# Kernel tuning notes

Measured on AMD Instinct MI355X. Metric: run time of the kernel, lower is better.

Reference implementation:

```python
import jax, jax.numpy as jnp
import numpy as np

N = 50000      # nodes
E = 800000     # edges (before self loops)
D_IN = 128
HID = 64
HEADS = 8
D_OUT = 10


def setup_inputs() -> dict:
    key = jax.random.key(0)
    ks = jax.random.split(key, 16)
    sc = 0.05
    x = jax.random.normal(ks[0], (N, D_IN), dtype=jnp.float32)
    edge_index = jax.random.randint(ks[1], (2, E), 0, N, dtype=jnp.int64)
    return {
        "x": x,
        "edge_index": edge_index,
        "W1": jax.random.normal(ks[2], (HEADS * HID, D_IN), dtype=jnp.float32) * sc,
        "a1_src": jax.random.normal(ks[3], (HEADS, HID), dtype=jnp.float32) * sc,
        "a1_dst": jax.random.normal(ks[4], (HEADS, HID), dtype=jnp.float32) * sc,
        "b1": jnp.zeros((HEADS * HID,), jnp.float32),
        "W2": jax.random.normal(ks[5], (HID, HEADS * HID), dtype=jnp.float32) * sc,
        "a2_src": jax.random.normal(ks[6], (1, HID), dtype=jnp.float32) * sc,
        "a2_dst": jax.random.normal(ks[7], (1, HID), dtype=jnp.float32) * sc,
        "b2": jnp.zeros((HID,), jnp.float32),
        "W3": jax.random.normal(ks[8], (HID, HID), dtype=jnp.float32) * sc,
        "a3_src": jax.random.normal(ks[9], (1, HID), dtype=jnp.float32) * sc,
        "a3_dst": jax.random.normal(ks[10], (1, HID), dtype=jnp.float32) * sc,
        "b3": jnp.zeros((HID,), jnp.float32),
        "Wc": jax.random.normal(ks[11], (D_OUT, HID), dtype=jnp.float32) * sc,
        "bc": jnp.zeros((D_OUT,), jnp.float32),
    }


def gat_conv(x, src, dst, W, a_src, a_dst, b, concat):
    """PyG GATConv (eval mode, add_self_loops already applied to src/dst)."""
    heads, out_ch = a_src.shape
    n = x.shape[0]
    h = (x @ W.T).reshape(n, heads, out_ch)          # [N, H, C]
    a_s = jnp.einsum('nhc,hc->nh', h, a_src)          # [N, H]
    a_d = jnp.einsum('nhc,hc->nh', h, a_dst)          # [N, H]
    e = jax.nn.leaky_relu(a_s[src] + a_d[dst], 0.2)   # [Etot, H]
    # segment softmax over incoming edges of each destination node
    m = jax.ops.segment_max(e, dst, num_segments=n)
    ex = jnp.exp(e - m[dst])
    s = jax.ops.segment_sum(ex, dst, num_segments=n)
    alpha = ex / (s[dst] + 1e-16)                     # [Etot, H]
    out = jax.ops.segment_sum(h[src] * alpha[:, :, None], dst, num_segments=n)
    if concat:
        out = out.reshape(n, heads * out_ch)
    else:
        out = out.mean(axis=1)
    return out + b


def reference(x, edge_index, W1, a1_src, a1_dst, b1, W2, a2_src, a2_dst, b2,
              W3, a3_src, a3_dst, b3, Wc, bc):
    loops = jnp.arange(N, dtype=edge_index.dtype)
    src = jnp.concatenate([edge_index[0], loops])
    dst = jnp.concatenate([edge_index[1], loops])
    h = jax.nn.elu(gat_conv(x, src, dst, W1, a1_src, a1_dst, b1, True))
    h = jax.nn.elu(gat_conv(h, src, dst, W2, a2_src, a2_dst, b2, False))
    h = jax.nn.elu(gat_conv(h, src, dst, W3, a3_src, a3_dst, b3, False))
    return h @ Wc.T + bc
```

## Files before the change

### kernel.cpp

```cpp
#include <hip/hip_runtime.h>
#include <math.h>

#define N_NODES 50000
#define N_EDGES 800000
#define ETOT    (N_EDGES + N_NODES)
#define COL_CAP (ETOT + 3 * N_NODES + 16)

typedef short bf16x8 __attribute__((ext_vector_type(8)));
typedef float f32x4  __attribute__((ext_vector_type(4)));
typedef float f32x2  __attribute__((ext_vector_type(2)));

__device__ __forceinline__ float b2f(unsigned int u16) {
    return __uint_as_float(u16 << 16);
}
__device__ __forceinline__ unsigned short f2b(float f) {
    unsigned int u = __float_as_uint(f);
    u += 0x7fffu + ((u >> 16) & 1u);
    return (unsigned short)(u >> 16);
}

__global__ __launch_bounds__(256) void k_prep(const float* __restrict__ x,
                                              const float* __restrict__ w1,
                                              const float* __restrict__ w2,
                                              const float* __restrict__ w3,
                                              unsigned short* __restrict__ xb,
                                              unsigned short* __restrict__ o1,
                                              unsigned short* __restrict__ o2,
                                              unsigned short* __restrict__ o3,
                                              int* __restrict__ deg,
                                              int* __restrict__ flag) {
    int i = blockIdx.x * 256 + threadIdx.x;
    if (i < N_NODES) deg[i] = 0;
    if (i == 0) *flag = 0;
    if (i < 512 * 128 / 4) {
        float4 v = ((const float4*)w1)[i];
        ushort2* o = (ushort2*)(o1 + i * 4);
        o[0] = make_ushort2(f2b(v.x), f2b(v.y));
        o[1] = make_ushort2(f2b(v.z), f2b(v.w));
    }
    if (i < 64 * 512 / 4) {
        float4 v = ((const float4*)w2)[i];
        ushort2* o = (ushort2*)(o2 + i * 4);
        o[0] = make_ushort2(f2b(v.x), f2b(v.y));
        o[1] = make_ushort2(f2b(v.z), f2b(v.w));
    }
    if (i < 64 * 64 / 4) {
        float4 v = ((const float4*)w3)[i];
        ushort2* o = (ushort2*)(o3 + i * 4);
        o[0] = make_ushort2(f2b(v.x), f2b(v.y));
        o[1] = make_ushort2(f2b(v.z), f2b(v.w));
    }
    if (i < N_NODES * 128 / 8) {
        const float4* xp = (const float4*)x + (size_t)i * 2;
        float4 v0 = xp[0], v1 = xp[1];
        unsigned int u0 = (unsigned int)f2b(v0.x) | ((unsigned int)f2b(v0.y) << 16);
        unsigned int u1 = (unsigned int)f2b(v0.z) | ((unsigned int)f2b(v0.w) << 16);
        unsigned int u2 = (unsigned int)f2b(v1.x) | ((unsigned int)f2b(v1.y) << 16);
        unsigned int u3 = (unsigned int)f2b(v1.z) | ((unsigned int)f2b(v1.w) << 16);
        *(uint4*)(xb + (size_t)i * 8) = make_uint4(u0, u1, u2, u3);
    }
}

__global__ void k_detect(const int* __restrict__ idx, int* __restrict__ flag) {
    int i = blockIdx.x * blockDim.x + threadIdx.x;
    int v = idx[2 * i + 1];
    unsigned long long any = __ballot(v != 0);
    if ((threadIdx.x & 63) == 0 && any) atomicOr(flag, 1);
}

__device__ __forceinline__ int edge_src(const int* idx, int e, int is32) {
    return is32 ? idx[e] : idx[2 * e];
}
__device__ __forceinline__ int edge_dst(const int* idx, int e, int is32) {
    return is32 ? idx[N_EDGES + e] : idx[2 * (N_EDGES + e)];
}

__global__ void k_degree(const int* __restrict__ idx, const int* __restrict__ flag,
                         int* __restrict__ deg) {
    int e = blockIdx.x * blockDim.x + threadIdx.x;
    if (e >= ETOT) return;
    int is32 = *flag;
    int d = (e < N_EDGES) ? edge_dst(idx, e, is32) : (e - N_EDGES);
    atomicAdd(&deg[d], 1);
}

__global__ __launch_bounds__(256) void k_scan1(const int* __restrict__ deg,
                                               int* __restrict__ rowptr,
                                               int* __restrict__ bsum) {
    __shared__ int sd[256];
    int t = threadIdx.x;
    int i = blockIdx.x * 256 + t;
    int v = (i < N_NODES) ? ((deg[i] + 3) & ~3) : 0;
    sd[t] = v;
    __syncthreads();
#pragma unroll
    for (int off = 1; off < 256; off <<= 1) {
        int a = (t >= off) ? sd[t - off] : 0;
        __syncthreads();
        sd[t] += a;
        __syncthreads();
    }
    if (i < N_NODES) rowptr[i] = sd[t] - v;
    if (t == 255) bsum[blockIdx.x] = sd[255];
}

__global__ __launch_bounds__(256) void k_scan2(int* __restrict__ bsum,
                                               int* __restrict__ boff,
                                               int* __restrict__ rowptr,
                                               int nb) {
    __shared__ int sd[256];
    int t = threadIdx.x;
    int v = (t < nb) ? bsum[t] : 0;
    sd[t] = v;
    __syncthreads();
#pragma unroll
    for (int off = 1; off < 256; off <<= 1) {
        int a = (t >= off) ? sd[t - off] : 0;
        __syncthreads();
        sd[t] += a;
        __syncthreads();
    }
    boff[t] = sd[t] - v;
    if (t == 255) rowptr[N_NODES] = sd[255];
}

__global__ __launch_bounds__(256) void k_scan3(int* __restrict__ rowptr,
                                               const int* __restrict__ boff,
                                               const int* __restrict__ deg,
                                               int* __restrict__ cursor,
                                               int* __restrict__ col) {
    int i = blockIdx.x * 256 + threadIdx.x;
    if (i == 0) {
        int tot = rowptr[N_NODES];
        for (int q = 0; q < 16; ++q) col[tot + q] = 0;
    }
    if (i >= N_NODES) return;
    int r = rowptr[i] + boff[blockIdx.x];
    rowptr[i] = r;
    cursor[i] = r;
    int d = deg[i];
    int pd = (d + 3) & ~3;
    for (int p = r + d; p < r + pd; ++p) col[p] = 0;
}

__global__ void k_scatter(const int* __restrict__ idx, const int* __restrict__ flag,
                          int* __restrict__ cursor, int* __restrict__ col) {
    int e = blockIdx.x * blockDim.x + threadIdx.x;
    if (e >= ETOT) return;
    int is32 = *flag;
    int s, d;
    if (e < N_EDGES) { s = edge_src(idx, e, is32); d = edge_dst(idx, e, is32); }
    else             { s = d = e - N_EDGES; }
    int pos = atomicAdd(&cursor[d], 1);
    col[pos] = s;
}

template<int AFP32>
__global__ __launch_bounds__(256) void k_gemm(const float* __restrict__ Af,
                                              const unsigned short* __restrict__ Ab,
                                              const unsigned short* __restrict__ W,
                                              unsigned short* __restrict__ C,
                                              const float* __restrict__ a_src,
                                              const float* __restrict__ a_dst,
                                              float* __restrict__ asb,
                                              float* __restrict__ adb,
                                              int M, int K, int Nout, int Hstr) {
    __shared__ unsigned short As[64 * 40];
    __shared__ unsigned short Bs[64 * 40];
    __shared__ float red_s[4][64];
    __shared__ float red_d[4][64];
    int t = threadIdx.x;
    int w = t >> 6, l = t & 63;
    int quad = l >> 4, lm = l & 15;
    int m0 = blockIdx.y * 64, n0 = blockIdx.x * 64;
    int hd = blockIdx.x;
    int lr = t >> 2;
    int lc = (t & 3) * 8;

    f32x4 acc[4];
#pragma unroll
    for (int r = 0; r < 4; ++r) acc[r] = (f32x4){0.f, 0.f, 0.f, 0.f};

    for (int k0 = 0; k0 < K; k0 += 32) {
        int m = m0 + lr;
        if (AFP32) {
            float4 a0 = {0.f,0.f,0.f,0.f}, a1 = {0.f,0.f,0.f,0.f};
            if (m < M) {
                const float4* ap = (const float4*)(Af + (size_t)m * K + k0 + lc);
                a0 = ap[0]; a1 = ap[1];
            }
            unsigned int u0 = (unsigned int)f2b(a0.x) | ((unsigned int)f2b(a0.y) << 16);
            unsigned int u1 = (unsigned int)f2b(a0.z) | ((unsigned int)f2b(a0.w) << 16);
            unsigned int u2 = (unsigned int)f2b(a1.x) | ((unsigned int)f2b(a1.y) << 16);
            unsigned int u3 = (unsigned int)f2b(a1.z) | ((unsigned int)f2b(a1.w) << 16);
            *(uint4*)&As[lr * 40 + lc] = make_uint4(u0, u1, u2, u3);
        } else {
            uint4 av = make_uint4(0, 0, 0, 0);
            if (m < M) av = *(const uint4*)(Ab + (size_t)m * K + k0 + lc);
            *(uint4*)&As[lr * 40 + lc] = av;
        }
        uint4 bv = *(const uint4*)(W + (size_t)(n0 + lr) * K + k0 + lc);
        *(uint4*)&Bs[lr * 40 + lc] = bv;
        __syncthreads();

        bf16x8 bfrag = *(const bf16x8*)&Bs[(w * 16 + lm) * 40 + quad * 8];
#pragma unroll
        for (int r = 0; r < 4; ++r) {
            bf16x8 afrag = *(const bf16x8*)&As[(r * 16 + lm) * 40 + quad * 8];
            acc[r] = __builtin_amdgcn_mfma_f32_16x16x32_bf16(afrag, bfrag, acc[r], 0, 0, 0);
        }
        __syncthreads();
    }

#pragma unroll
    for (int r = 0; r < 4; ++r)
#pragma unroll
        for (int g = 0; g < 4; ++g) {
            int m = m0 + r * 16 + quad * 4 + g;
            if (m < M) C[(size_t)m * Nout + n0 + w * 16 + lm] = f2b(acc[r][g]);
        }

    float as = a_src[hd * 64 + w * 16 + lm];
    float ad = a_dst[hd * 64 + w * 16 + lm];
#pragma unroll
    for (int r = 0; r < 4; ++r) {
#pragma unroll
        for (int g = 0; g < 4; ++g) {
            float vs = acc[r][g] * as;
            float vd = acc[r][g] * ad;
#pragma unroll
            for (int off = 1; off < 16; off <<= 1) {
                vs += __shfl_xor(vs, off);
                vd += __shfl_xor(vd, off);
            }
            if (lm == 0) {
                red_s[w][r * 16 + quad * 4 + g] = vs;
                red_d[w][r * 16 + quad * 4 + g] = vd;
            }
        }
    }
    __syncthreads();
    if (t < 64) {
        float vs = red_s[0][t] + red_s[1][t] + red_s[2][t] + red_s[3][t];
        float vd = red_d[0][t] + red_d[1][t] + red_d[2][t] + red_d[3][t];
        int m = m0 + t;
        if (m < M) {
            asb[(size_t)m * Hstr + hd] = vs;
            adb[(size_t)m * Hstr + hd] = vd;
        }
    }
}

__global__ __launch_bounds__(256) void k_agg8(const unsigned short* __restrict__ h,
                                              const float* __restrict__ asrc,
                                              const float* __restrict__ adst,
                                              const int* __restrict__ rowptr,
                                              const int* __restrict__ degv,
                                              const int* __restrict__ col,
                                              const float* __restrict__ bias,
                                              unsigned short* __restrict__ out) {
    int n = blockIdx.x * 4 + (threadIdx.x >> 6);
    if (n >= N_NODES) return;
    int l = threadIdx.x & 63;
    int j = l >> 3;
    unsigned lbase = (unsigned)(l << 3);
    int start = rowptr[n];
    int end   = start + degv[n];
    float adn = adst[((unsigned)n << 3) + (unsigned)j];

    float ssum = 0.f;
    f32x2 o2[4];
#pragma unroll
    for (int i = 0; i < 4; ++i) o2[i] = (f32x2){0.f, 0.f};

    float tA0, tA1, tA2, tA3, tB0, tB1, tB2, tB3;
    uint4 hA0, hA1, hA2, hA3, hB0, hB1, hB2, hB3;
    int4 cA, cB;

#define GATH8(c, T0, T1, T2, T3, H0, H1, H2, H3)                              \
    T0 = asrc[(((unsigned)(c).x) << 3) + (unsigned)j];                        \
    T1 = asrc[(((unsigned)(c).y) << 3) + (unsigned)j];                        \
    T2 = asrc[(((unsigned)(c).z) << 3) + (unsigned)j];                        \
    T3 = asrc[(((unsigned)(c).w) << 3) + (unsigned)j];                        \
    H0 = *(const uint4*)(h + (((unsigned)(c).x) << 9) + lbase);               \
    H1 = *(const uint4*)(h + (((unsigned)(c).y) << 9) + lbase);               \
    H2 = *(const uint4*)(h + (((unsigned)(c).z) << 9) + lbase);               \
    H3 = *(const uint4*)(h + (((unsigned)(c).w) << 9) + lbase);

#define ASLOT8(IDX, TT, HH, rem)                                              \
    {                                                                         \
        float e = TT + adn;                                                   \
        e = fmaxf(e, 0.2f * e);                                               \
        float ex = __expf(e);                                                 \
        ex = ((IDX) < (rem)) ? ex : 0.f;                                      \
        ssum += ex;                                                           \
        f32x2 ex2 = {ex, ex};                                                 \
        f32x2 f;                                                              \
        f.x = __uint_as_float((HH).x << 16);                                  \
        f.y = __uint_as_float((HH).x & 0xffff0000u);                          \
        asm("v_pk_fma_f32 %0, %1, %2, %0" : "+v"(o2[0]) : "v"(f), "v"(ex2));  \
        f.x = __uint_as_float((HH).y << 16);                                  \
        f.y = __uint_as_float((HH).y & 0xffff0000u);                          \
        asm("v_pk_fma_f32 %0, %1, %2, %0" : "+v"(o2[1]) : "v"(f), "v"(ex2));  \
        f.x = __uint_as_float((HH).z << 16);                                  \
        f.y = __uint_as_float((HH).z & 0xffff0000u);                          \
        asm("v_pk_fma_f32 %0, %1, %2, %0" : "+v"(o2[2]) : "v"(f), "v"(ex2));  \
        f.x = __uint_as_float((HH).w << 16);                                  \
        f.y = __uint_as_float((HH).w & 0xffff0000u);                          \
        asm("v_pk_fma_f32 %0, %1, %2, %0" : "+v"(o2[3]) : "v"(f), "v"(ex2));  \
    }

    int k = start;
    cA = *(const int4*)(col + k);
    cB = *(const int4*)(col + k + 4);
    GATH8(cA, tA0, tA1, tA2, tA3, hA0, hA1, hA2, hA3);
    for (;;) {
        bool hasB = (k + 4 < end);
        if (hasB) {
            GATH8(cB, tB0, tB1, tB2, tB3, hB0, hB1, hB2, hB3);
            cA = *(const int4*)(col + k + 8);
        }
        {
            int rem = end - k;
            ASLOT8(0, tA0, hA0, rem);
            ASLOT8(1, tA1, hA1, rem);
            ASLOT8(2, tA2, hA2, rem);
            ASLOT8(3, tA3, hA3, rem);
        }
        k += 4;
        if (!hasB) break;
        bool hasA = (k + 4 < end);
        if (hasA) {
            GATH8(cA, tA0, tA1, tA2, tA3, hA0, hA1, hA2, hA3);
            cB = *(const int4*)(col + k + 8);
        }
        {
            int rem = end - k;
            ASLOT8(0, tB0, hB0, rem);
            ASLOT8(1, tB1, hB1, rem);
            ASLOT8(2, tB2, hB2, rem);
            ASLOT8(3, tB3, hB3, rem);
        }
        k += 4;
        if (!hasA) break;
    }
#undef GATH8
#undef ASLOT8

    float inv = 1.f / (ssum + 1e-16f);
    unsigned int p[4];
#pragma unroll
    for (int i = 0; i < 4; ++i) {
        float v0 = o2[i].x * inv + bias[lbase + 2 * i];
        float v1 = o2[i].y * inv + bias[lbase + 2 * i + 1];
        v0 = (v0 > 0.f) ? v0 : expm1f(v0);
        v1 = (v1 > 0.f) ? v1 : expm1f(v1);
        p[i] = (unsigned int)f2b(v0) | ((unsigned int)f2b(v1) << 16);
    }
    *(uint4*)(out + (size_t)n * 512 + lbase) = make_uint4(p[0], p[1], p[2], p[3]);
}

__global__ __launch_bounds__(256) void k_agg1(const unsigned short* __restrict__ h,
                                              const float* __restrict__ asrc,
                                              const float* __restrict__ adst,
                                              const int* __restrict__ rowptr,
                                              const int* __restrict__ degv,
                                              const int* __restrict__ col,
                                              const float* __restrict__ bias,
                                              unsigned short* __restrict__ out) {
    int n = blockIdx.x * 4 + (threadIdx.x >> 6);
    if (n >= N_NODES) return;
    int l = threadIdx.x & 63;
    int start = rowptr[n];
    int end   = start + degv[n];
    float adn = adst[n];

    float ssum = 0.f, o = 0.f;
    float tA0, tA1, tA2, tA3, tB0, tB1, tB2, tB3;
    unsigned short qA0, qA1, qA2, qA3, qB0, qB1, qB2, qB3;
    int4 cA, cB;

#define GATH1(c, T0, T1, T2, T3, Q0, Q1, Q2, Q3)                              \
    T0 = asrc[(unsigned)(c).x];                                               \
    T1 = asrc[(unsigned)(c).y];                                               \
    T2 = asrc[(unsigned)(c).z];                                               \
    T3 = asrc[(unsigned)(c).w];                                               \
    Q0 = h[(((unsigned)(c).x) << 6) + (unsigned)l];                           \
    Q1 = h[(((unsigned)(c).y) << 6) + (unsigned)l];                           \
    Q2 = h[(((unsigned)(c).z) << 6) + (unsigned)l];                           \
    Q3 = h[(((unsigned)(c).w) << 6) + (unsigned)l];

#define ASLOT1(IDX, TT, QQ, rem)                                              \
    {                                                                         \
        float e = TT + adn;                                                   \
        e = fmaxf(e, 0.2f * e);                                               \
        float ex = __expf(e);                                                 \
        ex = ((IDX) < (rem)) ? ex : 0.f;                                      \
        ssum += ex;                                                           \
        o += ex * b2f(QQ);                                                    \
    }

    int k = start;
    cA = *(const int4*)(col + k);
    cB = *(const int4*)(col + k + 4);
    GATH1(cA, tA0, tA1, tA2, tA3, qA0, qA1, qA2, qA3);
    for (;;) {
        bool hasB = (k + 4 < end);
        if (hasB) {
            GATH1(cB, tB0, tB1, tB2, tB3, qB0, qB1, qB2, qB3);
            cA = *(const int4*)(col + k + 8);
        }
        {
            int rem = end - k;
            ASLOT1(0, tA0, qA0, rem);
            ASLOT1(1, tA1, qA1, rem);
            ASLOT1(2, tA2, qA2, rem);
            ASLOT1(3, tA3, qA3, rem);
        }
        k += 4;
        if (!hasB) break;
        bool hasA = (k + 4 < end);
        if (hasA) {
            GATH1(cA, tA0, tA1, tA2, tA3, qA0, qA1, qA2, qA3);
            cB = *(const int4*)(col + k + 8);
        }
        {
            int rem = end - k;
            ASLOT1(0, tB0, qB0, rem);
            ASLOT1(1, tB1, qB1, rem);
            ASLOT1(2, tB2, qB2, rem);
            ASLOT1(3, tB3, qB3, rem);
        }
        k += 4;
        if (!hasA) break;
    }
#undef GATH1
#undef ASLOT1

    float v = o / (ssum + 1e-16f) + bias[l];
    v = (v > 0.f) ? v : expm1f(v);
    out[(size_t)n * 64 + l] = f2b(v);
}

__global__ __launch_bounds__(256) void k_classifier(const unsigned short* __restrict__ h,
                                                    const float* __restrict__ Wc,
                                                    const float* __restrict__ bc,
                                                    float* __restrict__ out) {
    __shared__ float sW[640];
    for (int i = threadIdx.x; i < 640; i += blockDim.x) sW[i] = Wc[i];
    __syncthreads();
    int idx = blockIdx.x * blockDim.x + threadIdx.x;
    if (idx >= N_NODES * 10) return;
    int n = idx / 10, d = idx - n * 10;
    const unsigned short* hr = h + (size_t)n * 64;
    const float* wr = sW + d * 64;
    float acc = 0.f;
#pragma unroll
    for (int c = 0; c < 64; ++c) acc += b2f(hr[c]) * wr[c];
    out[idx] = acc + bc[d];
}

extern "C" void kernel_launch(void* const* d_in, const int* in_sizes, int n_in,
                              void* d_out, int out_size, void* d_ws, size_t ws_size,
                              hipStream_t stream) {
    const float* x    = (const float*)d_in[0];
    const int*   eidx = (const int*)  d_in[1];
    const float* W1   = (const float*)d_in[2];
    const float* a1s  = (const float*)d_in[3];
    const float* a1d  = (const float*)d_in[4];
    const float* b1   = (const float*)d_in[5];
    const float* W2   = (const float*)d_in[6];
    const float* a2s  = (const float*)d_in[7];
    const float* a2d  = (const float*)d_in[8];
    const float* b2   = (const float*)d_in[9];
    const float* W3   = (const float*)d_in[10];
    const float* a3s  = (const float*)d_in[11];
    const float* a3d  = (const float*)d_in[12];
    const float* b3   = (const float*)d_in[13];
    const float* Wc   = (const float*)d_in[14];
    const float* bc   = (const float*)d_in[15];
    float* out = (float*)d_out;

    float* asbuf = (float*)d_ws;
    float* adbuf = asbuf + (size_t)N_NODES * 8;
    unsigned short* h1  = (unsigned short*)(adbuf + (size_t)N_NODES * 8);
    unsigned short* x2  = h1  + (size_t)N_NODES * 512;
    unsigned short* h2  = x2  + (size_t)N_NODES * 512;
    unsigned short* x3  = h2  + (size_t)N_NODES * 64;
    unsigned short* h3  = x3  + (size_t)N_NODES * 64;
    unsigned short* x4  = h3  + (size_t)N_NODES * 64;
    unsigned short* xb  = x4  + (size_t)N_NODES * 64;
    unsigned short* W1b = xb  + (size_t)N_NODES * 128;
    unsigned short* W2b = W1b + 512 * 128;
    unsigned short* W3b = W2b + 64 * 512;
    int* ibase  = (int*)(W3b + 64 * 64);
    int* deg    = ibase;
    int* flag   = deg + N_NODES;
    int* rowptr = flag + 1;
    int* cursor = rowptr + N_NODES + 1;
    int* bsum   = cursor + N_NODES;
    int* boff   = bsum + 256;
    int* col    = boff + 256;

    dim3 blk(256);
    const int SCAN_BLOCKS = (N_NODES + 255) / 256;
    const int PREP_BLOCKS = (N_NODES * 128 / 8 + 255) / 256;

    k_prep<<<PREP_BLOCKS, blk, 0, stream>>>(x, W1, W2, W3, xb, W1b, W2b, W3b, deg, flag);
    k_detect<<<32, blk, 0, stream>>>(eidx, flag);
    k_degree<<<(ETOT + 255) / 256, blk, 0, stream>>>(eidx, flag, deg);
    k_scan1<<<SCAN_BLOCKS, blk, 0, stream>>>(deg, rowptr, bsum);
    k_scan2<<<1, blk, 0, stream>>>(bsum, boff, rowptr, SCAN_BLOCKS);
    k_scan3<<<SCAN_BLOCKS, blk, 0, stream>>>(rowptr, boff, deg, cursor, col);
    k_scatter<<<(ETOT + 255) / 256, blk, 0, stream>>>(eidx, flag, cursor, col);

    int mblocks = (N_NODES + 63) / 64;
    int nblocks = N_NODES / 4;

    k_gemm<0><<<dim3(8, mblocks), blk, 0, stream>>>((const float*)0, xb, W1b, h1,
                                                    a1s, a1d, asbuf, adbuf,
                                                    N_NODES, 128, 512, 8);
    k_agg8<<<nblocks, blk, 0, stream>>>(h1, asbuf, adbuf, rowptr, deg, col, b1, x2);

    k_gemm<0><<<dim3(1, mblocks), blk, 0, stream>>>((const float*)0, x2, W2b, h2,
                                                    a2s, a2d, asbuf, adbuf,
                                                    N_NODES, 512, 64, 1);
    k_agg1<<<nblocks, blk, 0, stream>>>(h2, asbuf, adbuf, rowptr, deg, col, b2, x3);

    k_gemm<0><<<dim3(1, mblocks), blk, 0, stream>>>((const float*)0, x3, W3b, h3,
                                                    a3s, a3d, asbuf, adbuf,
                                                    N_NODES, 64, 64, 1);
    k_agg1<<<nblocks, blk, 0, stream>>>(h3, asbuf, adbuf, rowptr, deg, col, b3, x4);

    k_classifier<<<(N_NODES * 10 + 255) / 256, blk, 0, stream>>>(x4, Wc, bc, out);
}
```

Before: 503.2 us.

## Aggregate raw inputs before layer-1 projection and fold attention vectors into W1

Layer 1 is reordered so attention logits come straight from the inputs, using precomputed U = a·W1 per head (k_prepu, k_attn). Edge aggregation then runs on the 128-wide bf16 inputs, giving a per-head aggregated matrix [N,8,128]. A per-head GEMM with fused bias and ELU follows, replacing the earlier GEMM plus 512-wide gather of h1. This cuts gather traffic per edge (256 bytes instead of 1 KB per edge) but writes a 1024-wide intermediate and changes rounding order.

```diff
diff --git a/kernel.cpp b/kernel.cpp
--- a/kernel.cpp
+++ b/kernel.cpp
@@ -61,6 +61,45 @@
     }
 }
 
+__global__ __launch_bounds__(256) void k_prepu(const float* __restrict__ W1,
+                                               const float* __restrict__ a1s,
+                                               const float* __restrict__ a1d,
+                                               float* __restrict__ U) {
+    int h = blockIdx.x;
+    int t = threadIdx.x;
+    int which = t >> 7, k = t & 127;
+    const float* av = which ? a1d : a1s;
+    float acc = 0.f;
+    for (int c = 0; c < 64; ++c)
+        acc += av[h * 64 + c] * W1[(size_t)(h * 64 + c) * 128 + k];
+    U[(which * 8 + h) * 128 + k] = acc;
+}
+
+__global__ __launch_bounds__(256) void k_attn(const unsigned short* __restrict__ xb,
+                                              const float* __restrict__ U,
+                                              float* __restrict__ asrc,
+                                              float* __restrict__ adst) {
+    __shared__ float sU[16 * 132];
+    __shared__ unsigned short sX[16 * 136];
+    int t = threadIdx.x;
+    for (int i = t; i < 2048; i += 256) sU[(i >> 7) * 132 + (i & 127)] = U[i];
+    int n0 = blockIdx.x * 16;
+    {
+        int r = t >> 4, c = (t & 15) * 8;
+        *(uint4*)&sX[r * 136 + c] = *(const uint4*)(xb + (size_t)(n0 + r) * 128 + c);
+    }
+    __syncthreads();
+    int nl = t >> 4, o = t & 15;
+    const unsigned short* xr = sX + nl * 136;
+    const float* ur = sU + o * 132;
+    float acc = 0.f;
+#pragma unroll 8
+    for (int k2 = 0; k2 < 128; ++k2) acc += b2f(xr[k2]) * ur[k2];
+    int n = n0 + nl;
+    if (o < 8) asrc[n * 8 + o] = acc;
+    else       adst[n * 8 + (o - 8)] = acc;
+}
+
 __global__ void k_detect(const int* __restrict__ idx, int* __restrict__ flag) {
     int i = blockIdx.x * blockDim.x + threadIdx.x;
     int v = idx[2 * i + 1];
@@ -155,16 +194,17 @@
     col[pos] = s;
 }
 
-template<int AFP32>
-__global__ __launch_bounds__(256) void k_gemm(const float* __restrict__ Af,
-                                              const unsigned short* __restrict__ Ab,
+template<int EPI>
+__global__ __launch_bounds__(256) void k_gemm(const unsigned short* __restrict__ Ab,
                                               const unsigned short* __restrict__ W,
                                               unsigned short* __restrict__ C,
                                               const float* __restrict__ a_src,
                                               const float* __restrict__ a_dst,
                                               float* __restrict__ asb,
                                               float* __restrict__ adb,
-                                              int M, int K, int Nout, int Hstr) {
+                                              const float* __restrict__ bias,
+                                              int M, int K, int Astr, int aoffmul,
+                                              int Nout, int Hstr) {
     __shared__ unsigned short As[64 * 40];
     __shared__ unsigned short Bs[64 * 40];
     __shared__ float red_s[4][64];
@@ -174,6 +214,7 @@
     int quad = l >> 4, lm = l & 15;
     int m0 = blockIdx.y * 64, n0 = blockIdx.x * 64;
     int hd = blockIdx.x;
+    int aoff = hd * aoffmul;
     int lr = t >> 2;
     int lc = (t & 3) * 8;
 
@@ -183,22 +224,9 @@
 
     for (int k0 = 0; k0 < K; k0 += 32) {
         int m = m0 + lr;
-        if (AFP32) {
-            float4 a0 = {0.f,0.f,0.f,0.f}, a1 = {0.f,0.f,0.f,0.f};
-            if (m < M) {
-                const float4* ap = (const float4*)(Af + (size_t)m * K + k0 + lc);
-                a0 = ap[0]; a1 = ap[1];
-            }
-            unsigned int u0 = (unsigned int)f2b(a0.x) | ((unsigned int)f2b(a0.y) << 16);
-            unsigned int u1 = (unsigned int)f2b(a0.z) | ((unsigned int)f2b(a0.w) << 16);
-            unsigned int u2 = (unsigned int)f2b(a1.x) | ((unsigned int)f2b(a1.y) << 16);
-            unsigned int u3 = (unsigned int)f2b(a1.z) | ((unsigned int)f2b(a1.w) << 16);
-            *(uint4*)&As[lr * 40 + lc] = make_uint4(u0, u1, u2, u3);
-        } else {
-            uint4 av = make_uint4(0, 0, 0, 0);
-            if (m < M) av = *(const uint4*)(Ab + (size_t)m * K + k0 + lc);
-            *(uint4*)&As[lr * 40 + lc] = av;
-        }
+        uint4 av = make_uint4(0, 0, 0, 0);
+        if (m < M) av = *(const uint4*)(Ab + (size_t)m * Astr + aoff + k0 + lc);
+        *(uint4*)&As[lr * 40 + lc] = av;
         uint4 bv = *(const uint4*)(W + (size_t)(n0 + lr) * K + k0 + lc);
         *(uint4*)&Bs[lr * 40 + lc] = bv;
         __syncthreads();
@@ -210,6 +238,22 @@
             acc[r] = __builtin_amdgcn_mfma_f32_16x16x32_bf16(afrag, bfrag, acc[r], 0, 0, 0);
         }
         __syncthreads();
+    }
+
+    if (EPI == 1) {
+        float bcol = bias[n0 + w * 16 + lm];
+#pragma unroll
+        for (int r = 0; r < 4; ++r)
+#pragma unroll
+            for (int g = 0; g < 4; ++g) {
+                int m = m0 + r * 16 + quad * 4 + g;
+                if (m < M) {
+                    float v = acc[r][g] + bcol;
+                    v = (v > 0.f) ? v : expm1f(v);
+                    C[(size_t)m * Nout + n0 + w * 16 + lm] = f2b(v);
+                }
+            }
+        return;
     }
 
 #pragma unroll
@@ -251,113 +295,104 @@
     }
 }
 
-__global__ __launch_bounds__(256) void k_agg8(const unsigned short* __restrict__ h,
+__device__ __forceinline__ void aggx_slot(int idx, int rem, float tt, unsigned int xx,
+                                          float adn, float& ssum, f32x2* acc) {
+    float e = tt + adn;
+    e = fmaxf(e, 0.2f * e);
+    float ex = __expf(e);
+    ex = (idx < rem) ? ex : 0.f;
+    ssum += ex;
+    float fx = __uint_as_float(xx << 16);
+    float fy = __uint_as_float(xx & 0xffff0000u);
+    int exi = __float_as_int(ex);
+#pragma unroll
+    for (int hh = 0; hh < 8; ++hh) {
+        float wh = __int_as_float(__builtin_amdgcn_readlane(exi, hh << 3));
+        acc[hh].x = fmaf(fx, wh, acc[hh].x);
+        acc[hh].y = fmaf(fy, wh, acc[hh].y);
+    }
+}
+
+__global__ __launch_bounds__(256) void k_aggx(const unsigned short* __restrict__ xb,
                                               const float* __restrict__ asrc,
                                               const float* __restrict__ adst,
                                               const int* __restrict__ rowptr,
                                               const int* __restrict__ degv,
                                               const int* __restrict__ col,
-                                              const float* __restrict__ bias,
-                                              unsigned short* __restrict__ out) {
+                                              unsigned short* __restrict__ aggX) {
     int n = blockIdx.x * 4 + (threadIdx.x >> 6);
     if (n >= N_NODES) return;
     int l = threadIdx.x & 63;
     int j = l >> 3;
-    unsigned lbase = (unsigned)(l << 3);
+    unsigned lx2 = (unsigned)(l << 1);
     int start = rowptr[n];
     int end   = start + degv[n];
     float adn = adst[((unsigned)n << 3) + (unsigned)j];
 
     float ssum = 0.f;
-    f32x2 o2[4];
-#pragma unroll
-    for (int i = 0; i < 4; ++i) o2[i] = (f32x2){0.f, 0.f};
+    f32x2 acc[8];
+#pragma unroll
+    for (int hh = 0; hh < 8; ++hh) acc[hh] = (f32x2){0.f, 0.f};
 
     float tA0, tA1, tA2, tA3, tB0, tB1, tB2, tB3;
-    uint4 hA0, hA1, hA2, hA3, hB0, hB1, hB2, hB3;
+    unsigned int xA0, xA1, xA2, xA3, xB0, xB1, xB2, xB3;
     int4 cA, cB;
 
-#define GATH8(c, T0, T1, T2, T3, H0, H1, H2, H3)                              \
+#define GATHX(c, T0, T1, T2, T3, X0, X1, X2, X3)                              \
     T0 = asrc[(((unsigned)(c).x) << 3) + (unsigned)j];                        \
     T1 = asrc[(((unsigned)(c).y) << 3) + (unsigned)j];                        \
     T2 = asrc[(((unsigned)(c).z) << 3) + (unsigned)j];                        \
     T3 = asrc[(((unsigned)(c).w) << 3) + (unsigned)j];                        \
-    H0 = *(const uint4*)(h + (((unsigned)(c).x) << 9) + lbase);               \
-    H1 = *(const uint4*)(h + (((unsigned)(c).y) << 9) + lbase);               \
-    H2 = *(const uint4*)(h + (((unsigned)(c).z) << 9) + lbase);               \
-    H3 = *(const uint4*)(h + (((unsigned)(c).w) << 9) + lbase);
-
-#define ASLOT8(IDX, TT, HH, rem)                                              \
-    {                                                                         \
-        float e = TT + adn;                                                   \
-        e = fmaxf(e, 0.2f * e);                                               \
-        float ex = __expf(e);                                                 \
-        ex = ((IDX) < (rem)) ? ex : 0.f;                                      \
-        ssum += ex;                                                           \
-        f32x2 ex2 = {ex, ex};                                                 \
-        f32x2 f;                                                              \
-        f.x = __uint_as_float((HH).x << 16);                                  \
-        f.y = __uint_as_float((HH).x & 0xffff0000u);                          \
-        asm("v_pk_fma_f32 %0, %1, %2, %0" : "+v"(o2[0]) : "v"(f), "v"(ex2));  \
-        f.x = __uint_as_float((HH).y << 16);                                  \
-        f.y = __uint_as_float((HH).y & 0xffff0000u);                          \
-        asm("v_pk_fma_f32 %0, %1, %2, %0" : "+v"(o2[1]) : "v"(f), "v"(ex2));  \
-        f.x = __uint_as_float((HH).z << 16);                                  \
-        f.y = __uint_as_float((HH).z & 0xffff0000u);                          \
-        asm("v_pk_fma_f32 %0, %1, %2, %0" : "+v"(o2[2]) : "v"(f), "v"(ex2));  \
-        f.x = __uint_as_float((HH).w << 16);                                  \
-        f.y = __uint_as_float((HH).w & 0xffff0000u);                          \
-        asm("v_pk_fma_f32 %0, %1, %2, %0" : "+v"(o2[3]) : "v"(f), "v"(ex2));  \
-    }
+    X0 = *(const unsigned int*)(xb + (((unsigned)(c).x) << 7) + lx2);         \
+    X1 = *(const unsigned int*)(xb + (((unsigned)(c).y) << 7) + lx2);         \
+    X2 = *(const unsigned int*)(xb + (((unsigned)(c).z) << 7) + lx2);         \
+    X3 = *(const unsigned int*)(xb + (((unsigned)(c).w) << 7) + lx2);
 
     int k = start;
     cA = *(const int4*)(col + k);
     cB = *(const int4*)(col + k + 4);
-    GATH8(cA, tA0, tA1, tA2, tA3, hA0, hA1, hA2, hA3);
+    GATHX(cA, tA0, tA1, tA2, tA3, xA0, xA1, xA2, xA3);
     for (;;) {
         bool hasB = (k + 4 < end);
         if (hasB) {
-            GATH8(cB, tB0, tB1, tB2, tB3, hB0, hB1, hB2, hB3);
+            GATHX(cB, tB0, tB1, tB2, tB3, xB0, xB1, xB2, xB3);
             cA = *(const int4*)(col + k + 8);
         }
         {
             int rem = end - k;
-            ASLOT8(0, tA0, hA0, rem);
-            ASLOT8(1, tA1, hA1, rem);
-            ASLOT8(2, tA2, hA2, rem);
-            ASLOT8(3, tA3, hA3, rem);
+            aggx_slot(0, rem, tA0, xA0, adn, ssum, acc);
+            aggx_slot(1, rem, tA1, xA1, adn, ssum, acc);
+            aggx_slot(2, rem, tA2, xA2, adn, ssum, acc);
+            aggx_slot(3, rem, tA3, xA3, adn, ssum, acc);
         }
         k += 4;
         if (!hasB) break;
         bool hasA = (k + 4 < end);
         if (hasA) {
-            GATH8(cA, tA0, tA1, tA2, tA3, hA0, hA1, hA2, hA3);
+            GATHX(cA, tA0, tA1, tA2, tA3, xA0, xA1, xA2, xA3);
             cB = *(const int4*)(col + k + 8);
         }
         {
             int rem = end - k;
-            ASLOT8(0, tB0, hB0, rem);
-            ASLOT8(1, tB1, hB1, rem);
-            ASLOT8(2, tB2, hB2, rem);
-            ASLOT8(3, tB3, hB3, rem);
+            aggx_slot(0, rem, tB0, xB0, adn, ssum, acc);
+            aggx_slot(1, rem, tB1, xB1, adn, ssum, acc);
+            aggx_slot(2, rem, tB2, xB2, adn, ssum, acc);
+            aggx_slot(3, rem, tB3, xB3, adn, ssum, acc);
         }
         k += 4;
         if (!hasA) break;
     }
-#undef GATH8
-#undef ASLOT8
-
-    float inv = 1.f / (ssum + 1e-16f);
-    unsigned int p[4];
-#pragma unroll
-    for (int i = 0; i < 4; ++i) {
-        float v0 = o2[i].x * inv + bias[lbase + 2 * i];
-        float v1 = o2[i].y * inv + bias[lbase + 2 * i + 1];
-        v0 = (v0 > 0.f) ? v0 : expm1f(v0);
-        v1 = (v1 > 0.f) ? v1 : expm1f(v1);
-        p[i] = (unsigned int)f2b(v0) | ((unsigned int)f2b(v1) << 16);
-    }
-    *(uint4*)(out + (size_t)n * 512 + lbase) = make_uint4(p[0], p[1], p[2], p[3]);
+#undef GATHX
+
+    size_t base = (size_t)n * 1024 + lx2;
+#pragma unroll
+    for (int hh = 0; hh < 8; ++hh) {
+        float sh = __int_as_float(__builtin_amdgcn_readlane(__float_as_int(ssum), hh << 3));
+        float iv = 1.f / (sh + 1e-16f);
+        unsigned int lo = f2b(acc[hh].x * iv);
+        unsigned int hi = f2b(acc[hh].y * iv);
+        *(unsigned int*)(aggX + base + hh * 128) = lo | (hi << 16);
+    }
 }
 
 __global__ __launch_bounds__(256) void k_agg1(const unsigned short* __restrict__ h,
@@ -483,17 +518,14 @@
 
     float* asbuf = (float*)d_ws;
     float* adbuf = asbuf + (size_t)N_NODES * 8;
-    unsigned short* h1  = (unsigned short*)(adbuf + (size_t)N_NODES * 8);
-    unsigned short* x2  = h1  + (size_t)N_NODES * 512;
-    unsigned short* h2  = x2  + (size_t)N_NODES * 512;
-    unsigned short* x3  = h2  + (size_t)N_NODES * 64;
-    unsigned short* h3  = x3  + (size_t)N_NODES * 64;
-    unsigned short* x4  = h3  + (size_t)N_NODES * 64;
-    unsigned short* xb  = x4  + (size_t)N_NODES * 64;
+    unsigned short* aggX = (unsigned short*)(adbuf + (size_t)N_NODES * 8);
+    unsigned short* x2  = aggX + (size_t)N_NODES * 1024;
+    unsigned short* xb  = x2  + (size_t)N_NODES * 512;
     unsigned short* W1b = xb  + (size_t)N_NODES * 128;
     unsigned short* W2b = W1b + 512 * 128;
     unsigned short* W3b = W2b + 64 * 512;
-    int* ibase  = (int*)(W3b + 64 * 64);
+    float* U    = (float*)(W3b + 64 * 64);
+    int* ibase  = (int*)(U + 16 * 128);
     int* deg    = ibase;
     int* flag   = deg + N_NODES;
     int* rowptr = flag + 1;
@@ -501,12 +533,19 @@
     int* bsum   = cursor + N_NODES;
     int* boff   = bsum + 256;
     int* col    = boff + 256;
+    unsigned short* h2 = aggX;
+    unsigned short* x3 = h2 + (size_t)N_NODES * 64;
+    unsigned short* h3 = x3 + (size_t)N_NODES * 64;
+    unsigned short* x4 = h3 + (size_t)N_NODES * 64;
 
     dim3 blk(256);
     const int SCAN_BLOCKS = (N_NODES + 255) / 256;
     const int PREP_BLOCKS = (N_NODES * 128 / 8 + 255) / 256;
 
     k_prep<<<PREP_BLOCKS, blk, 0, stream>>>(x, W1, W2, W3, xb, W1b, W2b, W3b, deg, flag);
+    k_prepu<<<8, blk, 0, stream>>>(W1, a1s, a1d, U);
+    k_attn<<<N_NODES / 16, blk, 0, stream>>>(xb, U, asbuf, adbuf);
+
     k_detect<<<32, blk, 0, stream>>>(eidx, flag);
     k_degree<<<(ETOT + 255) / 256, blk, 0, stream>>>(eidx, flag, deg);
     k_scan1<<<SCAN_BLOCKS, blk, 0, stream>>>(deg, rowptr, bsum);
@@ -517,19 +556,20 @@
     int mblocks = (N_NODES + 63) / 64;
     int nblocks = N_NODES / 4;
 
-    k_gemm<0><<<dim3(8, mblocks), blk, 0, stream>>>((const float*)0, xb, W1b, h1,
-                                                    a1s, a1d, asbuf, adbuf,
-                                                    N_NODES, 128, 512, 8);
-    k_agg8<<<nblocks, blk, 0, stream>>>(h1, asbuf, adbuf, rowptr, deg, col, b1, x2);
-
-    k_gemm<0><<<dim3(1, mblocks), blk, 0, stream>>>((const float*)0, x2, W2b, h2,
-                                                    a2s, a2d, asbuf, adbuf,
-                                                    N_NODES, 512, 64, 1);
+    k_aggx<<<nblocks, blk, 0, stream>>>(xb, asbuf, adbuf, rowptr, deg, col, aggX);
+    k_gemm<1><<<dim3(8, mblocks), blk, 0, stream>>>(aggX, W1b, x2,
+                                                    (const float*)0, (const float*)0,
+                                                    (float*)0, (float*)0, b1,
+                                                    N_NODES, 128, 1024, 128, 512, 8);
+
+    k_gemm<0><<<dim3(1, mblocks), blk, 0, stream>>>(x2, W2b, h2,
+                                                    a2s, a2d, asbuf, adbuf, (const float*)0,
+                                                    N_NODES, 512, 512, 0, 64, 1);
     k_agg1<<<nblocks, blk, 0, stream>>>(h2, asbuf, adbuf, rowptr, deg, col, b2, x3);
 
-    k_gemm<0><<<dim3(1, mblocks), blk, 0, stream>>>((const float*)0, x3, W3b, h3,
-                                                    a3s, a3d, asbuf, adbuf,
-                                                    N_NODES, 64, 64, 1);
+    k_gemm<0><<<dim3(1, mblocks), blk, 0, stream>>>(x3, W3b, h3,
+                                                    a3s, a3d, asbuf, adbuf, (const float*)0,
+                                                    N_NODES, 64, 64, 0, 64, 1);
     k_agg1<<<nblocks, blk, 0, stream>>>(h3, asbuf, adbuf, rowptr, deg, col, b3, x4);
 
     k_classifier<<<(N_NODES * 10 + 255) / 256, blk, 0, stream>>>(x4, Wc, bc, out);
```

Result: faster. 436.7 us (-13.2%).
